# Kernel tuning notes

Hardware: AMD Instinct MI355X
Metric: run time of the kernel (lower is better)

Reference implementation:

```python
import jax, jax.numpy as jnp
import numpy as np

N_NODES = 100000
N_EDGES = 1600000
IN_F = 128
H_F = 128
N_CLS = 8
N_LAYERS = 6


def setup_inputs() -> dict:
    key = jax.random.key(0)
    ks = jax.random.split(key, 8)
    scale = 1.0 / np.sqrt(H_F)
    return {
        "in_feat": jax.random.normal(ks[0], (N_NODES, IN_F), dtype=jnp.float32),
        "src": jax.random.randint(ks[1], (N_EDGES,), 0, N_NODES, dtype=jnp.int32),
        "dst": jax.random.randint(ks[2], (N_EDGES,), 0, N_NODES, dtype=jnp.int32),
        "edge_weight": jax.random.uniform(ks[3], (N_EDGES,), dtype=jnp.float32),
        "conv_W": jax.random.normal(ks[4], (N_LAYERS, H_F, H_F), dtype=jnp.float32) * scale,
        "conv_b": jnp.zeros((N_LAYERS, H_F), dtype=jnp.float32),
        "lin_W": jax.random.normal(ks[5], (H_F, N_CLS), dtype=jnp.float32) * scale,
        "lin_b": jnp.zeros((N_CLS,), dtype=jnp.float32),
    }


def _degree_norms(src, dst, n):
    ones = jnp.ones(src.shape[0], dtype=jnp.float32)
    out_deg = jax.ops.segment_sum(ones, src, num_segments=n)
    in_deg = jax.ops.segment_sum(ones, dst, num_segments=n)
    # DGL norm='both': clamp degrees to min 1, then ^-0.5 (structural degrees)
    norm_src = jnp.power(jnp.maximum(out_deg, 1.0), -0.5)[:, None]  # [N,1]
    norm_dst = jnp.power(jnp.maximum(in_deg, 1.0), -0.5)[:, None]   # [N,1]
    return norm_src, norm_dst


def _graph_conv(x, W, b, src, dst, ew, norm_src, norm_dst):
    # linear commutes with (linear) aggregation; apply weight first
    h = (x @ W) * norm_src                     # [N,F]
    msg = h[src] * ew[:, None]                 # [E,F] gather * edge weight
    agg = jax.ops.segment_sum(msg, dst, num_segments=x.shape[0])
    return agg * norm_dst + b


def reference(in_feat, src, dst, edge_weight, conv_W, conv_b, lin_W, lin_b):
    norm_src, norm_dst = _degree_norms(src, dst, in_feat.shape[0])
    h = in_feat
    for i in range(N_LAYERS):
        h = jax.nn.leaky_relu(
            _graph_conv(h, conv_W[i], conv_b[i], src, dst, edge_weight, norm_src, norm_dst),
            negative_slope=0.01,
        )
    return h @ lin_W + lin_b
```

## Files before the change

### kernel.cpp

```cpp
#include <hip/hip_runtime.h>
#include <math.h>

#define N_NODES 100000
#define N_EDGES 1600000
#define HF 128
#define N_CLS 8
#define N_LAYERS 6
#define TILE_N 64
#define SCAN_B 1024
#define SCAN_NB ((N_NODES + SCAN_B - 1) / SCAN_B)

__global__ void deg_kernel(const int* __restrict__ src, const int* __restrict__ dst,
                           int* __restrict__ outd, int* __restrict__ ind) {
    int e = blockIdx.x * blockDim.x + threadIdx.x;
    if (e < N_EDGES) {
        atomicAdd(&outd[src[e]], 1);
        atomicAdd(&ind[dst[e]], 1);
    }
}

__global__ void norm_kernel(const int* __restrict__ outd, const int* __restrict__ ind,
                            float* __restrict__ ns, float* __restrict__ nd) {
    int n = blockIdx.x * blockDim.x + threadIdx.x;
    if (n < N_NODES) {
        int od = outd[n]; if (od < 1) od = 1;
        int id = ind[n];  if (id < 1) id = 1;
        ns[n] = rsqrtf((float)od);
        nd[n] = rsqrtf((float)id);
    }
}

__global__ __launch_bounds__(SCAN_B) void scan1_kernel(const int* __restrict__ deg,
                                                       int* __restrict__ incl,
                                                       int* __restrict__ bsum) {
    __shared__ int buf[SCAN_B];
    int t = threadIdx.x;
    int g = blockIdx.x * SCAN_B + t;
    int v = (g < N_NODES) ? deg[g] : 0;
    buf[t] = v;
    __syncthreads();
    #pragma unroll
    for (int off = 1; off < SCAN_B; off <<= 1) {
        int add = (t >= off) ? buf[t - off] : 0;
        __syncthreads();
        buf[t] += add;
        __syncthreads();
    }
    if (g < N_NODES) incl[g] = buf[t];
    if (t == SCAN_B - 1) bsum[blockIdx.x] = buf[t];
}

__global__ __launch_bounds__(128) void scan2_kernel(int* __restrict__ bsum) {
    __shared__ int buf[128];
    int t = threadIdx.x;
    buf[t] = (t < SCAN_NB) ? bsum[t] : 0;
    __syncthreads();
    #pragma unroll
    for (int off = 1; off < 128; off <<= 1) {
        int add = (t >= off) ? buf[t - off] : 0;
        __syncthreads();
        buf[t] += add;
        __syncthreads();
    }
    if (t < SCAN_NB) bsum[t] = buf[t];
}

__global__ __launch_bounds__(SCAN_B) void scan3_kernel(const int* __restrict__ deg,
                                                       const int* __restrict__ incl,
                                                       const int* __restrict__ bsum,
                                                       int* __restrict__ row_ptr) {
    int t = threadIdx.x;
    int g = blockIdx.x * SCAN_B + t;
    if (g < N_NODES) {
        int off = (blockIdx.x > 0) ? bsum[blockIdx.x - 1] : 0;
        row_ptr[g] = off + incl[g] - deg[g];
    }
    if (g == 0) row_ptr[N_NODES] = bsum[SCAN_NB - 1];
}

__global__ void scatter_kernel(const int* __restrict__ src, const int* __restrict__ dst,
                               const float* __restrict__ ew, const int* __restrict__ row_ptr,
                               int* __restrict__ cursor, int* __restrict__ es,
                               float* __restrict__ ews) {
    int e = blockIdx.x * blockDim.x + threadIdx.x;
    if (e < N_EDGES) {
        int d = dst[e];
        int pos = row_ptr[d] + atomicAdd(&cursor[d], 1);
        es[pos] = src[e];
        ews[pos] = ew[e];
    }
}

__global__ __launch_bounds__(256) void gemm_kernel(const float* __restrict__ X,
                                                   const float* __restrict__ W,
                                                   const float* __restrict__ norm_src,
                                                   float* __restrict__ Y) {
    __shared__ float Xs[TILE_N][HF];
    int tid = threadIdx.x;
    int nodeBase = blockIdx.x * TILE_N;

    for (int i = tid; i < TILE_N * (HF / 4); i += 256) {
        int r = i >> 5;
        int c = i & 31;
        int n = nodeBase + r;
        float4 v = make_float4(0.f, 0.f, 0.f, 0.f);
        if (n < N_NODES) v = ((const float4*)(X + (size_t)n * HF))[c];
        ((float4*)(&Xs[r][0]))[c] = v;
    }
    __syncthreads();

    int tx = tid & 31;
    int ty = tid >> 5;

    float acc[8][4];
    #pragma unroll
    for (int i = 0; i < 8; i++)
        #pragma unroll
        for (int j = 0; j < 4; j++) acc[i][j] = 0.f;

    const float4* W4 = (const float4*)W;

    for (int k4 = 0; k4 < HF / 4; k4++) {
        float4 wv0 = W4[(k4 * 4 + 0) * 32 + tx];
        float4 wv1 = W4[(k4 * 4 + 1) * 32 + tx];
        float4 wv2 = W4[(k4 * 4 + 2) * 32 + tx];
        float4 wv3 = W4[(k4 * 4 + 3) * 32 + tx];
        #pragma unroll
        for (int i = 0; i < 8; i++) {
            float4 xv = ((const float4*)(&Xs[ty + 8 * i][0]))[k4];
            acc[i][0] += xv.x * wv0.x; acc[i][1] += xv.x * wv0.y;
            acc[i][2] += xv.x * wv0.z; acc[i][3] += xv.x * wv0.w;
            acc[i][0] += xv.y * wv1.x; acc[i][1] += xv.y * wv1.y;
            acc[i][2] += xv.y * wv1.z; acc[i][3] += xv.y * wv1.w;
            acc[i][0] += xv.z * wv2.x; acc[i][1] += xv.z * wv2.y;
            acc[i][2] += xv.z * wv2.z; acc[i][3] += xv.z * wv2.w;
            acc[i][0] += xv.w * wv3.x; acc[i][1] += xv.w * wv3.y;
            acc[i][2] += xv.w * wv3.z; acc[i][3] += xv.w * wv3.w;
        }
    }

    #pragma unroll
    for (int i = 0; i < 8; i++) {
        int n = nodeBase + ty + 8 * i;
        if (n < N_NODES) {
            float ns = norm_src[n];
            float4 o = make_float4(acc[i][0] * ns, acc[i][1] * ns,
                                   acc[i][2] * ns, acc[i][3] * ns);
            ((float4*)(Y + (size_t)n * HF))[tx] = o;
        }
    }
}

__global__ __launch_bounds__(256) void agg_kernel(const float* __restrict__ hl,
                                                  const int* __restrict__ row_ptr,
                                                  const int* __restrict__ es,
                                                  const float* __restrict__ ews,
                                                  const float* __restrict__ norm_dst,
                                                  const float* __restrict__ bias,
                                                  float* __restrict__ out) {
    int node = blockIdx.x * (blockDim.x >> 6) + (threadIdx.x >> 6);
    if (node >= N_NODES) return;
    int lane = threadIdx.x & 63;

    float ax = 0.f, ay = 0.f;
    int beg = row_ptr[node];
    int end = row_ptr[node + 1];
    int i = beg;
    for (; i + 2 <= end; i += 2) {
        int s0 = es[i];     int s1 = es[i + 1];
        float w0 = ews[i];  float w1 = ews[i + 1];
        float2 v0 = *(const float2*)(hl + (size_t)s0 * HF + lane * 2);
        float2 v1 = *(const float2*)(hl + (size_t)s1 * HF + lane * 2);
        ax += v0.x * w0; ay += v0.y * w0;
        ax += v1.x * w1; ay += v1.y * w1;
    }
    if (i < end) {
        int s = es[i];
        float w = ews[i];
        float2 v = *(const float2*)(hl + (size_t)s * HF + lane * 2);
        ax += v.x * w; ay += v.y * w;
    }
    float nd = norm_dst[node];
    float2 bb = *(const float2*)(bias + lane * 2);
    float ox = ax * nd + bb.x;
    float oy = ay * nd + bb.y;
    ox = (ox > 0.f) ? ox : 0.01f * ox;
    oy = (oy > 0.f) ? oy : 0.01f * oy;
    *(float2*)(out + (size_t)node * HF + lane * 2) = make_float2(ox, oy);
}

__global__ __launch_bounds__(256) void proj_kernel(const float* __restrict__ h,
                                                   const float* __restrict__ W,
                                                   const float* __restrict__ b,
                                                   float* __restrict__ out) {
    int node = blockIdx.x * (blockDim.x >> 6) + (threadIdx.x >> 6);
    if (node >= N_NODES) return;
    int lane = threadIdx.x & 63;

    float2 v = *(const float2*)(h + (size_t)node * HF + lane * 2);
    float acc[N_CLS];
    #pragma unroll
    for (int c = 0; c < N_CLS; c++) {
        acc[c] = v.x * W[(lane * 2) * N_CLS + c] + v.y * W[(lane * 2 + 1) * N_CLS + c];
    }
    #pragma unroll
    for (int off = 32; off > 0; off >>= 1) {
        #pragma unroll
        for (int c = 0; c < N_CLS; c++) acc[c] += __shfl_down(acc[c], off);
    }
    if (lane == 0) {
        #pragma unroll
        for (int c = 0; c < N_CLS; c++) out[(size_t)node * N_CLS + c] = acc[c] + b[c];
    }
}

extern "C" void kernel_launch(void* const* d_in, const int* in_sizes, int n_in,
                              void* d_out, int out_size, void* d_ws, size_t ws_size,
                              hipStream_t stream) {
    const float* in_feat = (const float*)d_in[0];
    const int*   src     = (const int*)d_in[1];
    const int*   dst     = (const int*)d_in[2];
    const float* ew      = (const float*)d_in[3];
    const float* conv_W  = (const float*)d_in[4];
    const float* conv_b  = (const float*)d_in[5];
    const float* lin_W   = (const float*)d_in[6];
    const float* lin_b   = (const float*)d_in[7];
    float* out = (float*)d_out;

    char* p = (char*)d_ws;
    float* hA = (float*)p;        p += (size_t)N_NODES * HF * sizeof(float);
    float* hB = (float*)p;        p += (size_t)N_NODES * HF * sizeof(float);
    int*   e_src = (int*)p;       p += (size_t)N_EDGES * sizeof(int);
    float* e_w = (float*)p;       p += (size_t)N_EDGES * sizeof(float);
    int*   row_ptr = (int*)p;     p += ((size_t)N_NODES + 8) * sizeof(int);
    int*   cursor = (int*)p;      p += (size_t)N_NODES * sizeof(int);
    int*   out_deg = (int*)p;     p += (size_t)N_NODES * sizeof(int);
    int*   in_deg = (int*)p;      p += (size_t)N_NODES * sizeof(int);
    float* norm_src = (float*)p;  p += (size_t)N_NODES * sizeof(float);
    float* norm_dst = (float*)p;  p += (size_t)N_NODES * sizeof(float);
    int*   incl = (int*)p;        p += (size_t)N_NODES * sizeof(int);
    int*   bsum = (int*)p;        p += 256 * sizeof(int);
    (void)p; (void)ws_size; (void)in_sizes; (void)n_in; (void)out_size;

    hipMemsetAsync(out_deg, 0, (size_t)N_NODES * sizeof(int), stream);
    hipMemsetAsync(in_deg, 0, (size_t)N_NODES * sizeof(int), stream);
    hipMemsetAsync(cursor, 0, (size_t)N_NODES * sizeof(int), stream);

    int egrid = (N_EDGES + 255) / 256;
    int ngrid = (N_NODES + 255) / 256;

    deg_kernel<<<egrid, 256, 0, stream>>>(src, dst, out_deg, in_deg);
    norm_kernel<<<ngrid, 256, 0, stream>>>(out_deg, in_deg, norm_src, norm_dst);
    scan1_kernel<<<SCAN_NB, SCAN_B, 0, stream>>>(in_deg, incl, bsum);
    scan2_kernel<<<1, 128, 0, stream>>>(bsum);
    scan3_kernel<<<SCAN_NB, SCAN_B, 0, stream>>>(in_deg, incl, bsum, row_ptr);
    scatter_kernel<<<egrid, 256, 0, stream>>>(src, dst, ew, row_ptr, cursor, e_src, e_w);

    int ggrid = (N_NODES + TILE_N - 1) / TILE_N;
    int agrid = (N_NODES + 3) / 4;

    const float* cur = in_feat;
    for (int l = 0; l < N_LAYERS; l++) {
        gemm_kernel<<<ggrid, 256, 0, stream>>>(cur, conv_W + (size_t)l * HF * HF,
                                               norm_src, hB);
        agg_kernel<<<agrid, 256, 0, stream>>>(hB, row_ptr, e_src, e_w, norm_dst,
                                              conv_b + (size_t)l * HF, hA);
        cur = hA;
    }
    proj_kernel<<<agrid, 256, 0, stream>>>(hA, lin_W, lin_b, out);
}
```

Baseline: 1.450 ms.

## Fold degree norms into edge weights and precompute CSR ranks in degree pass

Multiplies norm_src[s] and norm_dst[d] into each CSR edge weight once during the scatter, which removes the per-layer norm scaling in the GEMM epilogue and in the aggregation. The in-degree pass now records each edge's atomic rank, so the scatter needs no second round of atomics and the cursor buffer and its memset go away. Out-degree counting moves to a shared-memory histogram kernel that reads src in binned chunks, in place of global atomics. This adds an extra full read of src per histogram chunk and reuses the hB buffer for ranks before the layers overwrite it.

```diff
diff --git a/kernel.cpp b/kernel.cpp
--- a/kernel.cpp
+++ b/kernel.cpp
@@ -9,13 +9,43 @@
 #define TILE_N 64
 #define SCAN_B 1024
 #define SCAN_NB ((N_NODES + SCAN_B - 1) / SCAN_B)
-
-__global__ void deg_kernel(const int* __restrict__ src, const int* __restrict__ dst,
-                           int* __restrict__ outd, int* __restrict__ ind) {
+#define HBINS 8192
+#define HCHUNK ((N_NODES + HBINS - 1) / HBINS)
+#define HSLICE 8
+
+__global__ void deg_rank_kernel(const int* __restrict__ dst,
+                                int* __restrict__ ind, int* __restrict__ rank) {
     int e = blockIdx.x * blockDim.x + threadIdx.x;
     if (e < N_EDGES) {
-        atomicAdd(&outd[src[e]], 1);
-        atomicAdd(&ind[dst[e]], 1);
+        rank[e] = atomicAdd(&ind[dst[e]], 1);
+    }
+}
+
+__global__ __launch_bounds__(1024) void outdeg_hist_kernel(const int* __restrict__ src,
+                                                           int* __restrict__ outd) {
+    __shared__ int hist[HBINS];
+    int chunk = blockIdx.x;
+    int slice = blockIdx.y;
+    int lo = chunk * HBINS;
+    int hi = lo + HBINS;
+    for (int i = threadIdx.x; i < HBINS; i += 1024) hist[i] = 0;
+    __syncthreads();
+    const int4* s4 = (const int4*)src;
+    const int n4 = N_EDGES / 4;
+    int per = (n4 + HSLICE - 1) / HSLICE;
+    int beg = slice * per;
+    int end = beg + per; if (end > n4) end = n4;
+    for (int i = beg + threadIdx.x; i < end; i += 1024) {
+        int4 v = s4[i];
+        if (v.x >= lo && v.x < hi) atomicAdd(&hist[v.x - lo], 1);
+        if (v.y >= lo && v.y < hi) atomicAdd(&hist[v.y - lo], 1);
+        if (v.z >= lo && v.z < hi) atomicAdd(&hist[v.z - lo], 1);
+        if (v.w >= lo && v.w < hi) atomicAdd(&hist[v.w - lo], 1);
+    }
+    __syncthreads();
+    for (int i = threadIdx.x; i < HBINS; i += 1024) {
+        int c = hist[i];
+        if (c != 0 && lo + i < N_NODES) atomicAdd(&outd[lo + i], c);
     }
 }
 
@@ -78,22 +108,23 @@
     if (g == 0) row_ptr[N_NODES] = bsum[SCAN_NB - 1];
 }
 
-__global__ void scatter_kernel(const int* __restrict__ src, const int* __restrict__ dst,
-                               const float* __restrict__ ew, const int* __restrict__ row_ptr,
-                               int* __restrict__ cursor, int* __restrict__ es,
-                               float* __restrict__ ews) {
+__global__ void scatter2_kernel(const int* __restrict__ src, const int* __restrict__ dst,
+                                const float* __restrict__ ew, const float* __restrict__ ns,
+                                const float* __restrict__ nd, const int* __restrict__ row_ptr,
+                                const int* __restrict__ rank, int* __restrict__ es,
+                                float* __restrict__ ews) {
     int e = blockIdx.x * blockDim.x + threadIdx.x;
     if (e < N_EDGES) {
+        int s = src[e];
         int d = dst[e];
-        int pos = row_ptr[d] + atomicAdd(&cursor[d], 1);
-        es[pos] = src[e];
-        ews[pos] = ew[e];
+        int pos = row_ptr[d] + rank[e];
+        es[pos] = s;
+        ews[pos] = ew[e] * ns[s] * nd[d];
     }
 }
 
 __global__ __launch_bounds__(256) void gemm_kernel(const float* __restrict__ X,
                                                    const float* __restrict__ W,
-                                                   const float* __restrict__ norm_src,
                                                    float* __restrict__ Y) {
     __shared__ float Xs[TILE_N][HF];
     int tid = threadIdx.x;
@@ -143,9 +174,7 @@
     for (int i = 0; i < 8; i++) {
         int n = nodeBase + ty + 8 * i;
         if (n < N_NODES) {
-            float ns = norm_src[n];
-            float4 o = make_float4(acc[i][0] * ns, acc[i][1] * ns,
-                                   acc[i][2] * ns, acc[i][3] * ns);
+            float4 o = make_float4(acc[i][0], acc[i][1], acc[i][2], acc[i][3]);
             ((float4*)(Y + (size_t)n * HF))[tx] = o;
         }
     }
@@ -155,7 +184,6 @@
                                                   const int* __restrict__ row_ptr,
                                                   const int* __restrict__ es,
                                                   const float* __restrict__ ews,
-                                                  const float* __restrict__ norm_dst,
                                                   const float* __restrict__ bias,
                                                   float* __restrict__ out) {
     int node = blockIdx.x * (blockDim.x >> 6) + (threadIdx.x >> 6);
@@ -180,10 +208,9 @@
         float2 v = *(const float2*)(hl + (size_t)s * HF + lane * 2);
         ax += v.x * w; ay += v.y * w;
     }
-    float nd = norm_dst[node];
     float2 bb = *(const float2*)(bias + lane * 2);
-    float ox = ax * nd + bb.x;
-    float oy = ay * nd + bb.y;
+    float ox = ax + bb.x;
+    float oy = ay + bb.y;
     ox = (ox > 0.f) ? ox : 0.01f * ox;
     oy = (oy > 0.f) ? oy : 0.01f * oy;
     *(float2*)(out + (size_t)node * HF + lane * 2) = make_float2(ox, oy);
@@ -233,37 +260,37 @@
     int*   e_src = (int*)p;       p += (size_t)N_EDGES * sizeof(int);
     float* e_w = (float*)p;       p += (size_t)N_EDGES * sizeof(float);
     int*   row_ptr = (int*)p;     p += ((size_t)N_NODES + 8) * sizeof(int);
-    int*   cursor = (int*)p;      p += (size_t)N_NODES * sizeof(int);
     int*   out_deg = (int*)p;     p += (size_t)N_NODES * sizeof(int);
     int*   in_deg = (int*)p;      p += (size_t)N_NODES * sizeof(int);
     float* norm_src = (float*)p;  p += (size_t)N_NODES * sizeof(float);
     float* norm_dst = (float*)p;  p += (size_t)N_NODES * sizeof(float);
     int*   incl = (int*)p;        p += (size_t)N_NODES * sizeof(int);
     int*   bsum = (int*)p;        p += 256 * sizeof(int);
+    int*   rank = (int*)hB;
     (void)p; (void)ws_size; (void)in_sizes; (void)n_in; (void)out_size;
 
     hipMemsetAsync(out_deg, 0, (size_t)N_NODES * sizeof(int), stream);
     hipMemsetAsync(in_deg, 0, (size_t)N_NODES * sizeof(int), stream);
-    hipMemsetAsync(cursor, 0, (size_t)N_NODES * sizeof(int), stream);
 
     int egrid = (N_EDGES + 255) / 256;
     int ngrid = (N_NODES + 255) / 256;
 
-    deg_kernel<<<egrid, 256, 0, stream>>>(src, dst, out_deg, in_deg);
+    deg_rank_kernel<<<egrid, 256, 0, stream>>>(dst, in_deg, rank);
+    outdeg_hist_kernel<<<dim3(HCHUNK, HSLICE), 1024, 0, stream>>>(src, out_deg);
     norm_kernel<<<ngrid, 256, 0, stream>>>(out_deg, in_deg, norm_src, norm_dst);
     scan1_kernel<<<SCAN_NB, SCAN_B, 0, stream>>>(in_deg, incl, bsum);
     scan2_kernel<<<1, 128, 0, stream>>>(bsum);
     scan3_kernel<<<SCAN_NB, SCAN_B, 0, stream>>>(in_deg, incl, bsum, row_ptr);
-    scatter_kernel<<<egrid, 256, 0, stream>>>(src, dst, ew, row_ptr, cursor, e_src, e_w);
+    scatter2_kernel<<<egrid, 256, 0, stream>>>(src, dst, ew, norm_src, norm_dst,
+                                               row_ptr, rank, e_src, e_w);
 
     int ggrid = (N_NODES + TILE_N - 1) / TILE_N;
     int agrid = (N_NODES + 3) / 4;
 
     const float* cur = in_feat;
     for (int l = 0; l < N_LAYERS; l++) {
-        gemm_kernel<<<ggrid, 256, 0, stream>>>(cur, conv_W + (size_t)l * HF * HF,
-                                               norm_src, hB);
-        agg_kernel<<<agrid, 256, 0, stream>>>(hB, row_ptr, e_src, e_w, norm_dst,
+        gemm_kernel<<<ggrid, 256, 0, stream>>>(cur, conv_W + (size_t)l * HF * HF, hB);
+        agg_kernel<<<agrid, 256, 0, stream>>>(hB, row_ptr, e_src, e_w,
                                               conv_b + (size_t)l * HF, hA);
         cur = hA;
     }
```

New measurement: 1.347 ms. 7.1% less time.
